# Kernel optimization log

Measured on AMD Instinct MI355X. Metric: run time of the kernel, lower is better.

## Reference

```python
import jax, jax.numpy as jnp
import numpy as np

B, L, D, H = 16, 1024, 1024, 16
HD = D // H  # head dim = 64


def setup_inputs() -> dict:
    rng = jax.random.key(0)
    ks = jax.random.split(rng, 12)
    s = 0.02
    return {
        "key": jax.random.normal(ks[0], (B, L, D), jnp.float32),
        "value": jax.random.normal(ks[1], (B, L, D), jnp.float32),
        "query": jax.random.normal(ks[2], (B, L, D), jnp.float32),
        "atten_masks": jax.random.randint(ks[3], (B, L, L), 0, 2, jnp.int32),
        "Wk": jax.random.normal(ks[4], (D, D), jnp.float32) * s,
        "bk": jnp.zeros((D,), jnp.float32),
        "Wq": jax.random.normal(ks[5], (D, D), jnp.float32) * s,
        "bq": jnp.zeros((D,), jnp.float32),
        "Wv": jax.random.normal(ks[6], (D, D), jnp.float32) * s,
        "bv": jnp.zeros((D,), jnp.float32),
        "Wp": jax.random.normal(ks[7], (D, D), jnp.float32) * s,
        "bp": jnp.zeros((D,), jnp.float32),
    }


def reference(key, value, query, atten_masks, Wk, bk, Wq, bq, Wv, bv, Wp, bp):
    # Linear projections (torch nn.Linear: x @ W^T + b)
    def lin(x, W, b):
        return x @ W.T + b

    # [B, L, D] -> [B, H, L, HD]
    def heads(x):
        return x.reshape(B, L, H, HD).transpose(0, 2, 1, 3)

    k = heads(lin(key, Wk, bk))
    q = heads(lin(query, Wq, bq))
    v = heads(lin(value, Wv, bv))

    scale = 1.0 / np.sqrt(HD).astype(np.float32)
    att = jnp.einsum("bhqd,bhkd->bhqk", q, k) * scale  # [B, H, L, L]
    att = jnp.where(atten_masks[:, None, :, :] == 0, -jnp.inf, att)
    att = jax.nn.softmax(att, axis=-1)

    y = jnp.einsum("bhqk,bhkd->bhqd", att, v)  # [B, H, L, HD]
    y = y.transpose(0, 2, 1, 3).reshape(B, L, D)
    return lin(y, Wp, bp)
```

## Files before the change

### kernel.cpp

```cpp
#include <hip/hip_runtime.h>

typedef __bf16 bf16_t;
typedef __bf16 bf16x4 __attribute__((ext_vector_type(4)));
typedef __bf16 bf16x8 __attribute__((ext_vector_type(8)));
typedef float f32x4 __attribute__((ext_vector_type(4)));
typedef float f32x16 __attribute__((ext_vector_type(16)));

__device__ __forceinline__ int swz(int row) { return (row ^ (row >> 3)) & 7; }
__device__ __forceinline__ int swz2(int row) { return (row ^ (row >> 2)) & 3; }

__device__ __forceinline__ f32x4 mfma16(bf16x8 a, bf16x8 b, f32x4 c) {
  return __builtin_amdgcn_mfma_f32_16x16x32_bf16(a, b, c, 0, 0, 0);
}
__device__ __forceinline__ f32x16 mfma32(bf16x8 a, bf16x8 b, f32x16 c) {
  return __builtin_amdgcn_mfma_f32_32x32x16_bf16(a, b, c, 0, 0, 0);
}

__device__ __forceinline__ void gl_lds16(const void* g, void* l) {
  __builtin_amdgcn_global_load_lds(
      (const __attribute__((address_space(1))) unsigned int*)g,
      (__attribute__((address_space(3))) unsigned int*)l, 16, 0, 0);
}

__global__ __launch_bounds__(256) void cvt_all_kernel(
    const float* __restrict__ key, const float* __restrict__ query,
    const float* __restrict__ value, const float* __restrict__ Wk,
    const float* __restrict__ Wq, const float* __restrict__ Wv,
    const float* __restrict__ Wp, const int* __restrict__ mask,
    bf16_t* __restrict__ I1, bf16_t* __restrict__ I2, bf16_t* __restrict__ I3,
    bf16_t* __restrict__ Wkb, bf16_t* __restrict__ Wqb,
    bf16_t* __restrict__ Wvb, bf16_t* __restrict__ Wpb,
    unsigned* __restrict__ mbits) {
  const int bid = blockIdx.x;
  if (bid >= 53248) {
    int idx = (bid - 53248) * 256 + threadIdx.x;
    const int4* src = (const int4*)(mask + (size_t)idx * 32);
    unsigned w = 0;
#pragma unroll
    for (int i = 0; i < 8; ++i) {
      int4 v = src[i];
      w |= (v.x != 0 ? 1u : 0u) << (i * 4 + 0);
      w |= (v.y != 0 ? 1u : 0u) << (i * 4 + 1);
      w |= (v.z != 0 ? 1u : 0u) << (i * 4 + 2);
      w |= (v.w != 0 ? 1u : 0u) << (i * 4 + 3);
    }
    mbits[idx] = w;
    return;
  }
  const float* s;
  bf16_t* d;
  int base;
  if (bid < 16384) { s = key; d = I1; base = bid; }
  else if (bid < 32768) { s = query; d = I2; base = bid - 16384; }
  else if (bid < 49152) { s = value; d = I3; base = bid - 32768; }
  else if (bid < 50176) { s = Wk; d = Wkb; base = bid - 49152; }
  else if (bid < 51200) { s = Wq; d = Wqb; base = bid - 50176; }
  else if (bid < 52224) { s = Wv; d = Wvb; base = bid - 51200; }
  else { s = Wp; d = Wpb; base = bid - 52224; }
  int i = base * 256 + threadIdx.x;
  float4 v = ((const float4*)s)[i];
  bf16x4 o;
  o[0] = (bf16_t)v.x; o[1] = (bf16_t)v.y; o[2] = (bf16_t)v.z; o[3] = (bf16_t)v.w;
  ((bf16x4*)d)[i] = o;
}

template <typename OT>
__device__ __forceinline__ void gemm256_body(const bf16_t* __restrict__ A,
                                             const bf16_t* __restrict__ W,
                                             const float* __restrict__ bias,
                                             OT* __restrict__ O) {
  __shared__ __align__(16) bf16_t As[2][256 * 32];
  __shared__ __align__(16) bf16_t Bs[2][256 * 32];

  const int t = threadIdx.x;
  const int lane = t & 63;
  const int wid = t >> 6;
  const int g = lane >> 4;
  const int lr = lane & 15;
  const int wm = wid >> 2, wn = wid & 3;
  const int lid = blockIdx.x;
  const int logical = (lid & 7) * 32 + (lid >> 3);
  const int m0 = (logical >> 2) * 256;
  const int n0 = (logical & 3) * 256;

  f32x4 acc[8][4] = {};

  auto STAGE = [&](int buf, int kb) {
#pragma unroll
    for (int rr = 0; rr < 2; ++rr) {
      int s = rr * 512 + t;
      int row = s >> 2, c = s & 3;
      gl_lds16(A + (size_t)(m0 + row) * 1024 + kb + (c ^ swz2(row)) * 8,
               &As[buf][(rr * 512 + wid * 64) * 8]);
      gl_lds16(W + (size_t)(n0 + row) * 1024 + kb + (c ^ swz2(row)) * 8,
               &Bs[buf][(rr * 512 + wid * 64) * 8]);
    }
  };

  STAGE(0, 0);
  __syncthreads();
  int cur = 0;

  for (int kb = 0; kb < 1024; kb += 32) {
    if (kb < 992) STAGE(cur ^ 1, kb + 32);

    bf16x8 a[8], b[4];
#pragma unroll
    for (int i = 0; i < 8; ++i) {
      int row = wm * 128 + i * 16 + lr;
      a[i] = *(const bf16x8*)&As[cur][row * 32 + ((g ^ swz2(row))) * 8];
    }
#pragma unroll
    for (int j = 0; j < 4; ++j) {
      int row = wn * 64 + j * 16 + lr;
      b[j] = *(const bf16x8*)&Bs[cur][row * 32 + ((g ^ swz2(row))) * 8];
    }
    __builtin_amdgcn_s_setprio(1);
#pragma unroll
    for (int i = 0; i < 8; ++i)
#pragma unroll
      for (int j = 0; j < 4; ++j)
        acc[i][j] = mfma16(a[i], b[j], acc[i][j]);
    __builtin_amdgcn_s_setprio(0);

    __syncthreads();
    cur ^= 1;
  }

  float bval[4];
#pragma unroll
  for (int j = 0; j < 4; ++j) bval[j] = bias[n0 + wn * 64 + j * 16 + lr];
#pragma unroll
  for (int i = 0; i < 8; ++i)
#pragma unroll
    for (int r = 0; r < 4; ++r) {
      int row = m0 + wm * 128 + i * 16 + g * 4 + r;
#pragma unroll
      for (int j = 0; j < 4; ++j) {
        int n = n0 + wn * 64 + j * 16 + lr;
        O[(size_t)row * 1024 + n] = (OT)(acc[i][j][r] + bval[j]);
      }
    }
}

__global__ __launch_bounds__(512, 2) void gemm256_qkv_kernel(
    const bf16_t* key, const bf16_t* query, const bf16_t* value,
    const bf16_t* Wkb, const bf16_t* Wqb, const bf16_t* Wvb, const float* bk,
    const float* bq, const float* bv, bf16_t* ko, bf16_t* qo, bf16_t* vo) {
  const bf16_t *A, *W;
  const float* bi;
  bf16_t* O;
  if (blockIdx.y == 0) { A = key; W = Wkb; bi = bk; O = ko; }
  else if (blockIdx.y == 1) { A = query; W = Wqb; bi = bq; O = qo; }
  else { A = value; W = Wvb; bi = bv; O = vo; }
  gemm256_body<bf16_t>(A, W, bi, O);
}

__global__ __launch_bounds__(512, 2) void gemm256_out_kernel(
    const bf16_t* __restrict__ A, const bf16_t* __restrict__ W,
    const float* __restrict__ b, float* __restrict__ O) {
  gemm256_body<float>(A, W, b, O);
}

__global__ __launch_bounds__(256) void transpose_v_kernel(
    const bf16_t* __restrict__ v_ws, bf16_t* __restrict__ vT) {
  __shared__ bf16_t T[64 * 66];
  const int kc = blockIdx.x, h = blockIdx.y, b = blockIdx.z;
  const int t = threadIdx.x;
  {
    int key = t >> 2, dblk = t & 3;
    const bf16_t* src =
        v_ws + ((size_t)(b * 1024 + kc * 64 + key)) * 1024 + h * 64 + dblk * 16;
    bf16x8 a0 = *(const bf16x8*)src;
    bf16x8 a1 = *(const bf16x8*)(src + 8);
    bf16_t* row = &T[key * 66 + dblk * 16];
#pragma unroll
    for (int j = 0; j < 4; ++j) {
      ((unsigned*)row)[j] = ((const unsigned*)&a0)[j];
      ((unsigned*)row)[j + 4] = ((const unsigned*)&a1)[j];
    }
  }
  __syncthreads();
  {
    int d = t >> 2, kcl = t & 3;
    bf16x8 o0, o1;
#pragma unroll
    for (int e = 0; e < 8; ++e) {
      o0[e] = T[(kcl * 16 + e) * 66 + d];
      o1[e] = T[(kcl * 16 + 8 + e) * 66 + d];
    }
    bf16_t* dst =
        vT + ((size_t)((b * 16 + h) * 64 + d)) * 1024 + kc * 64 + kcl * 16;
    *(bf16x8*)dst = o0;
    *(bf16x8*)(dst + 8) = o1;
  }
}

#define ATTN_M2 10.0f

__global__ __launch_bounds__(256) void attn_kernel(
    const bf16_t* __restrict__ q_ws, const bf16_t* __restrict__ k_ws,
    const bf16_t* __restrict__ vT, const unsigned* __restrict__ mbits,
    bf16_t* __restrict__ y_ws) {
  __shared__ __align__(16) bf16_t Ks[64 * 64];
  __shared__ __align__(16) bf16_t Vs[64 * 64];
  __shared__ __align__(16) bf16_t Ps[4][32 * 64];

  const int lid = blockIdx.x;
  const int logical = (lid & 7) * 256 + (lid >> 3);
  const int qb = logical & 7;
  const int h = (logical >> 3) & 15;
  const int b = logical >> 7;
  const int t = threadIdx.x, lane = t & 63, wid = t >> 6;
  const int ql = lane & 31;
  const int hh = lane >> 5;
  const int q = qb * 128 + wid * 32 + ql;

  bf16x8 qf[4];
  {
    const bf16_t* qp = q_ws + ((size_t)(b * 1024 + q)) * 1024 + h * 64 + hh * 8;
#pragma unroll
    for (int kc = 0; kc < 4; ++kc) {
      bf16x8 raw = *(const bf16x8*)(qp + kc * 16);
      bf16x8 sc;
#pragma unroll
      for (int e = 0; e < 8; ++e)
        sc[e] = (bf16_t)((float)raw[e] * 0.18033688f);
      qf[kc] = sc;
    }
  }

  float l = 0.f;
  f32x16 acc0 = {}, acc1 = {};
  const bf16_t* Kb = k_ws + ((size_t)b * 1024) * 1024 + h * 64;
  const bf16_t* Vb = vT + ((size_t)((b * 16 + h) * 64)) * 1024;
  const unsigned* mrow = mbits + ((size_t)(b * 1024 + q)) * 32;

  for (int kb = 0; kb < 16; ++kb) {
    __syncthreads();
#pragma unroll
    for (int rr = 0; rr < 2; ++rr) {
      int s = rr * 256 + t;
      int row = s >> 3, c = s & 7;
      gl_lds16(Kb + (size_t)(kb * 64 + row) * 1024 + (c ^ swz(row)) * 8,
               &Ks[(rr * 256 + wid * 64) * 8]);
      gl_lds16(Vb + (size_t)row * 1024 + kb * 64 + (c ^ swz(row)) * 8,
               &Vs[(rr * 256 + wid * 64) * 8]);
    }
    uint2 mw = *(const uint2*)&mrow[kb * 2];
    __syncthreads();

    f32x16 c0 = {}, c1 = {};
    __builtin_amdgcn_s_setprio(1);
#pragma unroll
    for (int kc = 0; kc < 4; ++kc) {
      int sl = kc * 2 + hh;
      {
        int row = ql;
        bf16x8 kf = *(const bf16x8*)&Ks[row * 64 + ((sl ^ swz(row))) * 8];
        c0 = mfma32(kf, qf[kc], c0);
      }
      {
        int row = 32 + ql;
        bf16x8 kf = *(const bf16x8*)&Ks[row * 64 + ((sl ^ swz(row))) * 8];
        c1 = mfma32(kf, qf[kc], c1);
      }
    }
    __builtin_amdgcn_s_setprio(0);

    unsigned wx = mw.x >> (4 * hh);
    unsigned wy = mw.y >> (4 * hh);
    float p0[16], p1[16];
    float ps = 0.f;
#pragma unroll
    for (int r = 0; r < 16; ++r) {
      const int posr = (r & 3) + 8 * (r >> 2);
      int n0m = (int)(wx << (31 - posr)) >> 31;
      int n1m = (int)(wy << (31 - posr)) >> 31;
      float e0 = __builtin_amdgcn_exp2f(c0[r] - ATTN_M2);
      float e1 = __builtin_amdgcn_exp2f(c1[r] - ATTN_M2);
      e0 = __int_as_float(__float_as_int(e0) & n0m);
      e1 = __int_as_float(__float_as_int(e1) & n1m);
      p0[r] = e0;
      p1[r] = e1;
      ps += e0 + e1;
    }
    ps += __shfl_xor(ps, 32);
    l += ps;

#pragma unroll
    for (int j = 0; j < 4; ++j) {
      bf16x4 w0, w1;
#pragma unroll
      for (int e = 0; e < 4; ++e) {
        w0[e] = (bf16_t)p0[4 * j + e];
        w1[e] = (bf16_t)p1[4 * j + e];
      }
      int off = 4 * hh;
      *(bf16x4*)&Ps[wid][ql * 64 + ((j ^ swz(ql)) * 8) + off] = w0;
      *(bf16x4*)&Ps[wid][ql * 64 + (((4 + j) ^ swz(ql)) * 8) + off] = w1;
    }
    bf16x8 pb[4];
#pragma unroll
    for (int kc = 0; kc < 4; ++kc) {
      int sl = kc * 2 + hh;
      pb[kc] = *(const bf16x8*)&Ps[wid][ql * 64 + ((sl ^ swz(ql))) * 8];
    }

    __builtin_amdgcn_s_setprio(1);
#pragma unroll
    for (int kc = 0; kc < 4; ++kc) {
      int sl = kc * 2 + hh;
      {
        int row = ql;
        bf16x8 vf = *(const bf16x8*)&Vs[row * 64 + ((sl ^ swz(row))) * 8];
        acc0 = mfma32(vf, pb[kc], acc0);
      }
      {
        int row = 32 + ql;
        bf16x8 vf = *(const bf16x8*)&Vs[row * 64 + ((sl ^ swz(row))) * 8];
        acc1 = mfma32(vf, pb[kc], acc1);
      }
    }
    __builtin_amdgcn_s_setprio(0);
  }

  float inv = 1.0f / fmaxf(l, 1e-30f);
  bf16_t* yp = y_ws + ((size_t)(b * 1024 + q)) * 1024 + h * 64;
#pragma unroll
  for (int j = 0; j < 4; ++j) {
    bf16x4 o0, o1;
#pragma unroll
    for (int e = 0; e < 4; ++e) {
      o0[e] = (bf16_t)(acc0[4 * j + e] * inv);
      o1[e] = (bf16_t)(acc1[4 * j + e] * inv);
    }
    *(bf16x4*)&yp[8 * j + 4 * hh] = o0;
    *(bf16x4*)&yp[32 + 8 * j + 4 * hh] = o1;
  }
}

extern "C" void kernel_launch(void* const* d_in, const int* in_sizes, int n_in,
                              void* d_out, int out_size, void* d_ws,
                              size_t ws_size, hipStream_t stream) {
  (void)in_sizes; (void)n_in; (void)out_size; (void)ws_size;
  const float* key = (const float*)d_in[0];
  const float* value = (const float*)d_in[1];
  const float* query = (const float*)d_in[2];
  const int* mask = (const int*)d_in[3];
  const float* Wk = (const float*)d_in[4];
  const float* bk = (const float*)d_in[5];
  const float* Wq = (const float*)d_in[6];
  const float* bq = (const float*)d_in[7];
  const float* Wv = (const float*)d_in[8];
  const float* bv = (const float*)d_in[9];
  const float* Wp = (const float*)d_in[10];
  const float* bp = (const float*)d_in[11];
  float* out = (float*)d_out;

  char* ws = (char*)d_ws;
  const size_t MB = 1ull << 20;
  unsigned* mbits = (unsigned*)(ws);
  bf16_t* Wkb = (bf16_t*)(ws + 2 * MB);
  bf16_t* Wqb = (bf16_t*)(ws + 4 * MB);
  bf16_t* Wvb = (bf16_t*)(ws + 6 * MB);
  bf16_t* Wpb = (bf16_t*)(ws + 8 * MB);
  bf16_t* I1 = (bf16_t*)(ws + 10 * MB);
  bf16_t* I2 = (bf16_t*)(ws + 42 * MB);
  bf16_t* I3 = (bf16_t*)(ws + 74 * MB);
  bf16_t* k_ws = (bf16_t*)(ws + 106 * MB);
  bf16_t* q_ws = (bf16_t*)(ws + 138 * MB);
  bf16_t* v_ws = (bf16_t*)(ws + 170 * MB);
  bf16_t* vT_ws = I1;
  bf16_t* y_ws = I2;

  cvt_all_kernel<<<55296, 256, 0, stream>>>(key, query, value, Wk, Wq, Wv, Wp,
                                            mask, I1, I2, I3, Wkb, Wqb, Wvb,
                                            Wpb, mbits);
  gemm256_qkv_kernel<<<dim3(256, 3), 512, 0, stream>>>(
      I1, I2, I3, Wkb, Wqb, Wvb, bk, bq, bv, k_ws, q_ws, v_ws);
  transpose_v_kernel<<<dim3(16, 16, 16), 256, 0, stream>>>(v_ws, vT_ws);
  attn_kernel<<<2048, 256, 0, stream>>>(q_ws, k_ws, vT_ws, mbits, y_ws);
  gemm256_out_kernel<<<256, 512, 0, stream>>>(y_ws, Wpb, bp, out);
}
```

Baseline: 374.1 us.

## Triple-buffer GEMM LDS stages with one barrier per k-step

Switches the projection GEMMs from double-buffered static LDS to triple-buffered dynamic LDS, prefetching two k-tiles ahead. Explicit vmcnt waits and a single raw barrier per iteration replace the trailing __syncthreads. The aim is to hide global-to-LDS load latency and cut synchronisation. It raises LDS use to 96KB per block, which may limit co-residency of blocks on a CU.

Measured after the change: 352.6 us. 1.06x faster.

```diff
diff --git a/kernel.cpp b/kernel.cpp
--- a/kernel.cpp
+++ b/kernel.cpp
@@ -69,8 +69,9 @@
                                              const bf16_t* __restrict__ W,
                                              const float* __restrict__ bias,
                                              OT* __restrict__ O) {
-  __shared__ __align__(16) bf16_t As[2][256 * 32];
-  __shared__ __align__(16) bf16_t Bs[2][256 * 32];
+  extern __shared__ __align__(16) char smem[];
+  bf16_t* AsBase = (bf16_t*)smem;
+  bf16_t* BsBase = (bf16_t*)(smem + 3 * 8192 * 2);
 
   const int t = threadIdx.x;
   const int lane = t & 63;
@@ -86,34 +87,50 @@
   f32x4 acc[8][4] = {};
 
   auto STAGE = [&](int buf, int kb) {
+    bf16_t* Ab = AsBase + buf * 8192;
+    bf16_t* Bb = BsBase + buf * 8192;
 #pragma unroll
     for (int rr = 0; rr < 2; ++rr) {
       int s = rr * 512 + t;
       int row = s >> 2, c = s & 3;
       gl_lds16(A + (size_t)(m0 + row) * 1024 + kb + (c ^ swz2(row)) * 8,
-               &As[buf][(rr * 512 + wid * 64) * 8]);
+               &Ab[(rr * 512 + wid * 64) * 8]);
       gl_lds16(W + (size_t)(n0 + row) * 1024 + kb + (c ^ swz2(row)) * 8,
-               &Bs[buf][(rr * 512 + wid * 64) * 8]);
+               &Bb[(rr * 512 + wid * 64) * 8]);
     }
   };
 
   STAGE(0, 0);
-  __syncthreads();
+  STAGE(1, 32);
+
   int cur = 0;
-
   for (int kb = 0; kb < 1024; kb += 32) {
-    if (kb < 992) STAGE(cur ^ 1, kb + 32);
-
+    if (kb + 32 < 1024)
+      asm volatile("s_waitcnt vmcnt(4)" ::: "memory");
+    else
+      asm volatile("s_waitcnt vmcnt(0)" ::: "memory");
+    __builtin_amdgcn_sched_barrier(0);
+    __builtin_amdgcn_s_barrier();
+    __builtin_amdgcn_sched_barrier(0);
+
+    if (kb + 64 < 1024) {
+      int fut = cur + 2;
+      if (fut >= 3) fut -= 3;
+      STAGE(fut, kb + 64);
+    }
+
+    const bf16_t* Ab = AsBase + cur * 8192;
+    const bf16_t* Bb = BsBase + cur * 8192;
     bf16x8 a[8], b[4];
 #pragma unroll
     for (int i = 0; i < 8; ++i) {
       int row = wm * 128 + i * 16 + lr;
-      a[i] = *(const bf16x8*)&As[cur][row * 32 + ((g ^ swz2(row))) * 8];
+      a[i] = *(const bf16x8*)&Ab[row * 32 + ((g ^ swz2(row))) * 8];
     }
 #pragma unroll
     for (int j = 0; j < 4; ++j) {
       int row = wn * 64 + j * 16 + lr;
-      b[j] = *(const bf16x8*)&Bs[cur][row * 32 + ((g ^ swz2(row))) * 8];
+      b[j] = *(const bf16x8*)&Bb[row * 32 + ((g ^ swz2(row))) * 8];
     }
     __builtin_amdgcn_s_setprio(1);
 #pragma unroll
@@ -123,8 +140,7 @@
         acc[i][j] = mfma16(a[i], b[j], acc[i][j]);
     __builtin_amdgcn_s_setprio(0);
 
-    __syncthreads();
-    cur ^= 1;
+    cur = (cur == 2) ? 0 : cur + 1;
   }
 
   float bval[4];
@@ -374,12 +390,14 @@
   bf16_t* vT_ws = I1;
   bf16_t* y_ws = I2;
 
+  const size_t GEMM_LDS = 3 * 8192 * 2 * 2;
+
   cvt_all_kernel<<<55296, 256, 0, stream>>>(key, query, value, Wk, Wq, Wv, Wp,
                                             mask, I1, I2, I3, Wkb, Wqb, Wvb,
                                             Wpb, mbits);
-  gemm256_qkv_kernel<<<dim3(256, 3), 512, 0, stream>>>(
+  gemm256_qkv_kernel<<<dim3(256, 3), 512, GEMM_LDS, stream>>>(
       I1, I2, I3, Wkb, Wqb, Wvb, bk, bq, bv, k_ws, q_ws, v_ws);
   transpose_v_kernel<<<dim3(16, 16, 16), 256, 0, stream>>>(v_ws, vT_ws);
   attn_kernel<<<2048, 256, 0, stream>>>(q_ws, k_ws, vT_ws, mbits, y_ws);
-  gemm256_out_kernel<<<256, 512, 0, stream>>>(y_ws, Wpb, bp, out);
-}
+  gemm256_out_kernel<<<256, 512, GEMM_LDS, stream>>>(y_ws, Wpb, bp, out);
+}
```
